# Kernel tuning notes

Measured on AMD Instinct MI355X. Metric: run time of the kernel, lower is better.

## Reference

```python
import jax, jax.numpy as jnp
import numpy as np

NUM_IMGS = 8192
NUM_CAPS = 8192
R = 7        # views per image
D = 256      # embedding dim


def setup_inputs() -> dict:
    key = jax.random.key(0)
    k1, k2 = jax.random.split(key)
    imgs = jax.random.normal(k1, (NUM_IMGS, R, D), dtype=jnp.float32)
    caps = jax.random.normal(k2, (NUM_CAPS, D), dtype=jnp.float32)
    return {"imgs": imgs, "caps": caps}


def reference(imgs, caps):
    # scores[i, r, c] = <imgs[i, r], caps[c]>  then max over views r
    # matches torch.matmul(imgs, caps.t()).max(1)[0]
    scores = jnp.einsum("ird,cd->irc", imgs, caps)  # [num_imgs, r, num_caps]
    return scores.max(axis=1)                        # [num_imgs, num_caps]
```

## Files before the change

### kernel.cpp

```cpp
#include <hip/hip_runtime.h>
#include <hip/hip_bf16.h>
#include <cstdint>
#include <cstddef>

#define NI 8192
#define NC 8192
#define RV 7
#define DD 256

typedef __bf16  bf16x8 __attribute__((ext_vector_type(8)));
typedef float   f32x4  __attribute__((ext_vector_type(4)));
typedef __fp16  f16x2  __attribute__((ext_vector_type(2)));

#define IMGS_WS_BYTES (16u * 56u * 32768u)
#define CAPS_WS_OFF   IMGS_WS_BYTES
#define CAPS_WS_BYTES (64u * 65536u)
#define WS_NEEDED     ((size_t)(IMGS_WS_BYTES + CAPS_WS_BYTES))

static __device__ __forceinline__ unsigned pkbf(float x, float y) {
  unsigned a = __float_as_uint(x) + 0x8000u;
  unsigned b = __float_as_uint(y) + 0x8000u;
  return __builtin_amdgcn_perm(b, a, 0x07060302u);
}

static __device__ __forceinline__ void gload16(const void* g, void* l) {
  __builtin_amdgcn_global_load_lds(
      (const __attribute__((address_space(1))) void*)g,
      (__attribute__((address_space(3))) void*)l, 16, 0, 0);
}

__global__ __launch_bounds__(256)
void conv_imgs(const float* __restrict__ imgs, uint4* __restrict__ ws) {
  unsigned T = blockIdx.x * 256u + threadIdx.x;
  unsigned img = T / 224u;
  unsigned rem = T - img * 224u;
  unsigned r  = rem >> 5;
  unsigned ju = rem & 31u;
  const float* s = imgs + ((size_t)img * RV + r) * DD + ju * 8u;
  float4 a = *(const float4*)s;
  float4 b = *(const float4*)(s + 4);
  uint4 v = { pkbf(a.x, a.y), pkbf(a.z, a.w), pkbf(b.x, b.y), pkbf(b.z, b.w) };
  unsigned ib = img >> 9, lrow = img & 511u;
  unsigned j = ju >> 2, u = ju & 3u;
  unsigned t = r * 8u + j;
  unsigned byteoff = (ib * 56u + t) * 32768u + u * 8192u + lrow * 16u;
  ws[byteoff >> 4] = v;
}

__global__ __launch_bounds__(256)
void conv_caps(const float* __restrict__ caps, uint4* __restrict__ ws) {
  unsigned T = blockIdx.x * 256u + threadIdx.x;
  unsigned gr = T >> 5;
  unsigned ju = T & 31u;
  const float* s = caps + (size_t)gr * DD + ju * 8u;
  float4 a = *(const float4*)s;
  float4 b = *(const float4*)(s + 4);
  uint4 v = { pkbf(a.x, a.y), pkbf(a.z, a.w), pkbf(b.x, b.y), pkbf(b.z, b.w) };
  unsigned cb = gr >> 7, row = gr & 127u;
  unsigned j = ju >> 2, u = ju & 3u;
  unsigned byteoff = cb * 65536u + j * 8192u + u * 2048u + row * 16u;
  ws[byteoff >> 4] = v;
}

__global__ __launch_bounds__(512, 2)
void mvm_mfma(const char* __restrict__ wi, const char* __restrict__ wcap,
              float* __restrict__ out)
{
  __shared__ __align__(1024) char lds[131072];
  char* const ldsA = lds;
  char* const ldsB = lds + 65536;

  const int tid  = threadIdx.x;
  const int lane = tid & 63;
  const int wid  = tid >> 6;
  const int wm   = wid >> 1;
  const int wn   = wid & 1;

  const int bid = (int)blockIdx.x;
  const int swz = (bid & 7) * 128 + (bid >> 3);
  const int ib  = swz >> 6;
  const int cb  = swz & 63;

  const char* abase = wi   + (size_t)ib * (56u * 32768u);
  const char* bbase = wcap + (size_t)cb * 65536u;

  #pragma unroll
  for (int l = 0; l < 8; ++l)
    gload16(bbase + l * 8192 + tid * 16, ldsB + l * 8192 + wid * 1024);
  #pragma unroll
  for (int l = 0; l < 4; ++l)
    gload16(abase + l * 8192 + tid * 16, ldsA + l * 8192 + wid * 1024);

  asm volatile("s_waitcnt vmcnt(0)" ::: "memory");
  __builtin_amdgcn_s_barrier();
  asm volatile("" ::: "memory");

  const int lrow = lane & 15;
  const int lu   = lane >> 4;
  const char* const aB = ldsA + lu * 8192 + (wm * 128 + lrow) * 16;
  const char* const bB = ldsB + lu * 2048 + (wn * 64  + lrow) * 16;
  const char* ap = abase + 32768 + tid * 16;

  f16x2 om[8][4][2];
  #pragma unroll
  for (int m = 0; m < 8; ++m)
    #pragma unroll
    for (int n = 0; n < 4; ++n)
      #pragma unroll
      for (int h = 0; h < 2; ++h)
        om[m][n][h] = (f16x2){(__fp16)-65504.f, (__fp16)-65504.f};

  f32x4 acc[8][4];

  for (int r = 0; r < RV; ++r) {
    #pragma unroll
    for (int m = 0; m < 8; ++m)
      #pragma unroll
      for (int n = 0; n < 4; ++n)
        acc[m][n] = (f32x4){0.f, 0.f, 0.f, 0.f};

    #pragma unroll
    for (int j = 0; j < 8; ++j) {
      const int p = j & 1;
      const bool more = (r < RV - 1) || (j < 7);

      if (more) {
        gload16(ap,         ldsA + (p ^ 1) * 32768 + 0 * 8192 + wid * 1024);
        gload16(ap +  8192, ldsA + (p ^ 1) * 32768 + 1 * 8192 + wid * 1024);
        gload16(ap + 16384, ldsA + (p ^ 1) * 32768 + 2 * 8192 + wid * 1024);
        gload16(ap + 24576, ldsA + (p ^ 1) * 32768 + 3 * 8192 + wid * 1024);
        ap += 32768;
      }

      bf16x8 b0 = *(const bf16x8*)(bB + j * 8192 + 0 * 256);
      bf16x8 b1 = *(const bf16x8*)(bB + j * 8192 + 1 * 256);
      bf16x8 b2 = *(const bf16x8*)(bB + j * 8192 + 2 * 256);
      bf16x8 b3 = *(const bf16x8*)(bB + j * 8192 + 3 * 256);
      bf16x8 a0 = *(const bf16x8*)(aB + p * 32768 + 0 * 256);
      bf16x8 a1 = *(const bf16x8*)(aB + p * 32768 + 1 * 256);
      bf16x8 a2 = *(const bf16x8*)(aB + p * 32768 + 2 * 256);
      bf16x8 a3 = *(const bf16x8*)(aB + p * 32768 + 3 * 256);
      bf16x8 a4 = *(const bf16x8*)(aB + p * 32768 + 4 * 256);
      bf16x8 a5 = *(const bf16x8*)(aB + p * 32768 + 5 * 256);
      bf16x8 a6 = *(const bf16x8*)(aB + p * 32768 + 6 * 256);
      bf16x8 a7 = *(const bf16x8*)(aB + p * 32768 + 7 * 256);

      __builtin_amdgcn_s_setprio(1);
      acc[0][0] = __builtin_amdgcn_mfma_f32_16x16x32_bf16(a0, b0, acc[0][0], 0, 0, 0);
      acc[1][0] = __builtin_amdgcn_mfma_f32_16x16x32_bf16(a1, b0, acc[1][0], 0, 0, 0);
      acc[2][0] = __builtin_amdgcn_mfma_f32_16x16x32_bf16(a2, b0, acc[2][0], 0, 0, 0);
      acc[3][0] = __builtin_amdgcn_mfma_f32_16x16x32_bf16(a3, b0, acc[3][0], 0, 0, 0);
      acc[4][0] = __builtin_amdgcn_mfma_f32_16x16x32_bf16(a4, b0, acc[4][0], 0, 0, 0);
      acc[5][0] = __builtin_amdgcn_mfma_f32_16x16x32_bf16(a5, b0, acc[5][0], 0, 0, 0);
      acc[6][0] = __builtin_amdgcn_mfma_f32_16x16x32_bf16(a6, b0, acc[6][0], 0, 0, 0);
      acc[7][0] = __builtin_amdgcn_mfma_f32_16x16x32_bf16(a7, b0, acc[7][0], 0, 0, 0);
      acc[0][1] = __builtin_amdgcn_mfma_f32_16x16x32_bf16(a0, b1, acc[0][1], 0, 0, 0);
      acc[1][1] = __builtin_amdgcn_mfma_f32_16x16x32_bf16(a1, b1, acc[1][1], 0, 0, 0);
      acc[2][1] = __builtin_amdgcn_mfma_f32_16x16x32_bf16(a2, b1, acc[2][1], 0, 0, 0);
      acc[3][1] = __builtin_amdgcn_mfma_f32_16x16x32_bf16(a3, b1, acc[3][1], 0, 0, 0);
      acc[4][1] = __builtin_amdgcn_mfma_f32_16x16x32_bf16(a4, b1, acc[4][1], 0, 0, 0);
      acc[5][1] = __builtin_amdgcn_mfma_f32_16x16x32_bf16(a5, b1, acc[5][1], 0, 0, 0);
      acc[6][1] = __builtin_amdgcn_mfma_f32_16x16x32_bf16(a6, b1, acc[6][1], 0, 0, 0);
      acc[7][1] = __builtin_amdgcn_mfma_f32_16x16x32_bf16(a7, b1, acc[7][1], 0, 0, 0);
      acc[0][2] = __builtin_amdgcn_mfma_f32_16x16x32_bf16(a0, b2, acc[0][2], 0, 0, 0);
      acc[1][2] = __builtin_amdgcn_mfma_f32_16x16x32_bf16(a1, b2, acc[1][2], 0, 0, 0);
      acc[2][2] = __builtin_amdgcn_mfma_f32_16x16x32_bf16(a2, b2, acc[2][2], 0, 0, 0);
      acc[3][2] = __builtin_amdgcn_mfma_f32_16x16x32_bf16(a3, b2, acc[3][2], 0, 0, 0);
      acc[4][2] = __builtin_amdgcn_mfma_f32_16x16x32_bf16(a4, b2, acc[4][2], 0, 0, 0);
      acc[5][2] = __builtin_amdgcn_mfma_f32_16x16x32_bf16(a5, b2, acc[5][2], 0, 0, 0);
      acc[6][2] = __builtin_amdgcn_mfma_f32_16x16x32_bf16(a6, b2, acc[6][2], 0, 0, 0);
      acc[7][2] = __builtin_amdgcn_mfma_f32_16x16x32_bf16(a7, b2, acc[7][2], 0, 0, 0);
      acc[0][3] = __builtin_amdgcn_mfma_f32_16x16x32_bf16(a0, b3, acc[0][3], 0, 0, 0);
      acc[1][3] = __builtin_amdgcn_mfma_f32_16x16x32_bf16(a1, b3, acc[1][3], 0, 0, 0);
      acc[2][3] = __builtin_amdgcn_mfma_f32_16x16x32_bf16(a2, b3, acc[2][3], 0, 0, 0);
      acc[3][3] = __builtin_amdgcn_mfma_f32_16x16x32_bf16(a3, b3, acc[3][3], 0, 0, 0);
      acc[4][3] = __builtin_amdgcn_mfma_f32_16x16x32_bf16(a4, b3, acc[4][3], 0, 0, 0);
      acc[5][3] = __builtin_amdgcn_mfma_f32_16x16x32_bf16(a5, b3, acc[5][3], 0, 0, 0);
      acc[6][3] = __builtin_amdgcn_mfma_f32_16x16x32_bf16(a6, b3, acc[6][3], 0, 0, 0);
      acc[7][3] = __builtin_amdgcn_mfma_f32_16x16x32_bf16(a7, b3, acc[7][3], 0, 0, 0);
      __builtin_amdgcn_s_setprio(0);

      if (more) {
        asm volatile("s_waitcnt vmcnt(0)" ::: "memory");
        __builtin_amdgcn_s_barrier();
        asm volatile("" ::: "memory");
      }
    }

    #pragma unroll
    for (int m = 0; m < 8; ++m)
      #pragma unroll
      for (int n = 0; n < 4; ++n) {
        f16x2 lo = __builtin_amdgcn_cvt_pkrtz(acc[m][n][0], acc[m][n][1]);
        f16x2 hi = __builtin_amdgcn_cvt_pkrtz(acc[m][n][2], acc[m][n][3]);
        om[m][n][0] = __builtin_elementwise_max(om[m][n][0], lo);
        om[m][n][1] = __builtin_elementwise_max(om[m][n][1], hi);
      }
  }

  const int rbase = ib * 512 + wm * 128;
  const int cbase = cb * 128 + wn * 64;
  #pragma unroll
  for (int m = 0; m < 8; ++m)
    #pragma unroll
    for (int h = 0; h < 2; ++h)
      #pragma unroll
      for (int e = 0; e < 2; ++e) {
        size_t ro = (size_t)(rbase + m * 16 + lu * 4 + h * 2 + e) * NC + cbase + lrow;
        #pragma unroll
        for (int n = 0; n < 4; ++n)
          out[ro + n * 16] = (float)om[m][n][h][e];
      }
}

__global__ __launch_bounds__(512, 1)
void mvm_fallback(const float* __restrict__ imgs, const float* __restrict__ caps,
                  float* __restrict__ out)
{
  __shared__ __align__(16) char ldsB[128 * 512];
  __shared__ __align__(16) char ldsA[2][256 * 128];

  const int tid  = threadIdx.x;
  const int lane = tid & 63;
  const int wid  = tid >> 6;
  const int wr   = wid >> 1;
  const int wc   = wid & 1;
  const int i0   = blockIdx.y * 256;
  const int c0   = blockIdx.x * 128;

  #pragma unroll
  for (int it = 0; it < 8; ++it) {
    int c    = tid + it * 512;
    int row  = c >> 5;
    int colb = (c & 31) * 16;
    const float* p = caps + (size_t)(c0 + row) * DD + (c & 31) * 8;
    float4 a = *(const float4*)p;
    float4 b = *(const float4*)(p + 4);
    uint4 v;
    v.x = pkbf(a.x, a.y); v.y = pkbf(a.z, a.w);
    v.z = pkbf(b.x, b.y); v.w = pkbf(b.z, b.w);
    *(uint4*)(ldsB + row * 512 + (colb ^ ((row & 7) << 4))) = v;
  }
  #pragma unroll
  for (int it = 0; it < 4; ++it) {
    int c    = tid + it * 512;
    int row  = c >> 3;
    int colb = (c & 7) * 16;
    const float* p = imgs + ((size_t)(i0 + row) * RV + 0) * DD + (c & 7) * 8;
    float4 a = *(const float4*)p;
    float4 b = *(const float4*)(p + 4);
    uint4 v;
    v.x = pkbf(a.x, a.y); v.y = pkbf(a.z, a.w);
    v.z = pkbf(b.x, b.y); v.w = pkbf(b.z, b.w);
    *(uint4*)(ldsA[0] + row * 128 + (colb ^ ((row & 7) << 4))) = v;
  }
  __syncthreads();

  f32x4 omax[4][4];
  #pragma unroll
  for (int m = 0; m < 4; ++m)
    #pragma unroll
    for (int n = 0; n < 4; ++n)
      #pragma unroll
      for (int j = 0; j < 4; ++j)
        omax[m][n][j] = -3.4e38f;

  f32x4 acc[4][4];
  int cur = 0;
  const int lrow = lane & 15;
  const int lkb  = (lane >> 4) * 16;

  for (int ch = 0; ch < RV * 4; ++ch) {
    const int kc = ch & 3;
    if (kc == 0) {
      #pragma unroll
      for (int m = 0; m < 4; ++m)
        #pragma unroll
        for (int n = 0; n < 4; ++n)
          acc[m][n] = (f32x4){0.f, 0.f, 0.f, 0.f};
    }
    const int  chn  = ch + 1;
    const bool hasn = (chn < RV * 4);
    float4 pf[8];
    if (hasn) {
      const int rn = chn >> 2;
      const int kn = (chn & 3) * 64;
      #pragma unroll
      for (int it = 0; it < 4; ++it) {
        int c   = tid + it * 512;
        int row = c >> 3;
        const float* p = imgs + ((size_t)(i0 + row) * RV + rn) * DD + kn + (c & 7) * 8;
        pf[2 * it]     = *(const float4*)p;
        pf[2 * it + 1] = *(const float4*)(p + 4);
      }
    }
    #pragma unroll
    for (int ks = 0; ks < 2; ++ks) {
      bf16x8 af[4], bfr[4];
      #pragma unroll
      for (int m = 0; m < 4; ++m) {
        int row = wr * 64 + m * 16 + lrow;
        af[m] = *(const bf16x8*)(ldsA[cur] + row * 128 + ((ks * 64 + lkb) ^ ((row & 7) << 4)));
      }
      #pragma unroll
      for (int n = 0; n < 4; ++n) {
        int row = wc * 64 + n * 16 + lrow;
        bfr[n] = *(const bf16x8*)(ldsB + row * 512 + (((ch & 3) * 128 + ks * 64 + lkb) ^ ((row & 7) << 4)));
      }
      #pragma unroll
      for (int m = 0; m < 4; ++m)
        #pragma unroll
        for (int n = 0; n < 4; ++n)
          acc[m][n] = __builtin_amdgcn_mfma_f32_16x16x32_bf16(af[m], bfr[n], acc[m][n], 0, 0, 0);
    }
    if (hasn) {
      #pragma unroll
      for (int it = 0; it < 4; ++it) {
        int c    = tid + it * 512;
        int row  = c >> 3;
        int colb = (c & 7) * 16;
        uint4 v;
        v.x = pkbf(pf[2 * it].x,     pf[2 * it].y);
        v.y = pkbf(pf[2 * it].z,     pf[2 * it].w);
        v.z = pkbf(pf[2 * it + 1].x, pf[2 * it + 1].y);
        v.w = pkbf(pf[2 * it + 1].z, pf[2 * it + 1].w);
        *(uint4*)(ldsA[cur ^ 1] + row * 128 + (colb ^ ((row & 7) << 4))) = v;
      }
    }
    __syncthreads();
    cur ^= 1;
    if (kc == 3) {
      #pragma unroll
      for (int m = 0; m < 4; ++m)
        #pragma unroll
        for (int n = 0; n < 4; ++n)
          #pragma unroll
          for (int j = 0; j < 4; ++j)
            omax[m][n][j] = fmaxf(omax[m][n][j], acc[m][n][j]);
    }
  }

  const int rbase = i0 + wr * 64;
  const int cbase = c0 + wc * 64;
  const int lr4   = (lane >> 4) * 4;
  const int lc    = lane & 15;
  #pragma unroll
  for (int m = 0; m < 4; ++m)
    #pragma unroll
    for (int j = 0; j < 4; ++j) {
      size_t ro = (size_t)(rbase + m * 16 + lr4 + j) * NC;
      #pragma unroll
      for (int n = 0; n < 4; ++n)
        out[ro + cbase + n * 16 + lc] = omax[m][n][j];
    }
}

extern "C" void kernel_launch(void* const* d_in, const int* in_sizes, int n_in,
                              void* d_out, int out_size, void* d_ws, size_t ws_size,
                              hipStream_t stream) {
  const float* imgs = (const float*)d_in[0];
  const float* caps = (const float*)d_in[1];
  float* out = (float*)d_out;

  if (ws_size >= WS_NEEDED) {
    char* ws = (char*)d_ws;
    conv_imgs<<<7168, 256, 0, stream>>>(imgs, (uint4*)ws);
    conv_caps<<<1024, 256, 0, stream>>>(caps, (uint4*)(ws + CAPS_WS_OFF));
    mvm_mfma<<<1024, 512, 0, stream>>>((const char*)ws, (const char*)(ws + CAPS_WS_OFF), out);
  } else {
    dim3 grid(NC / 128, NI / 256);
    mvm_fallback<<<grid, 512, 0, stream>>>(imgs, caps, out);
  }
}
```

Baseline: 258.8 us.

## Load image operand directly from global into registers, dropping LDS staging

The image (A) tiles are no longer copied into a double-buffered LDS region. Each wave now reads its A fragments straight from the pre-packed global workspace into registers, prefetching the next chunk in two halves between MFMA groups. This removes the per-chunk vmcnt wait and block barrier, and halves the LDS footprint, which may allow two blocks per CU. In exchange, the two waves sharing the same rows duplicate global reads and rely on caches. Load latency is hidden only by a single register-level prefetch stage, and the final prefetch reads past the tile into the next region.

```diff
diff --git a/kernel.cpp b/kernel.cpp
--- a/kernel.cpp
+++ b/kernel.cpp
@@ -66,9 +66,7 @@
 void mvm_mfma(const char* __restrict__ wi, const char* __restrict__ wcap,
               float* __restrict__ out)
 {
-  __shared__ __align__(1024) char lds[131072];
-  char* const ldsA = lds;
-  char* const ldsB = lds + 65536;
+  __shared__ __align__(1024) char ldsB[65536];
 
   const int tid  = threadIdx.x;
   const int lane = tid & 63;
@@ -87,19 +85,24 @@
   #pragma unroll
   for (int l = 0; l < 8; ++l)
     gload16(bbase + l * 8192 + tid * 16, ldsB + l * 8192 + wid * 1024);
-  #pragma unroll
-  for (int l = 0; l < 4; ++l)
-    gload16(abase + l * 8192 + tid * 16, ldsA + l * 8192 + wid * 1024);
-
   asm volatile("s_waitcnt vmcnt(0)" ::: "memory");
   __builtin_amdgcn_s_barrier();
   asm volatile("" ::: "memory");
 
   const int lrow = lane & 15;
   const int lu   = lane >> 4;
-  const char* const aB = ldsA + lu * 8192 + (wm * 128 + lrow) * 16;
-  const char* const bB = ldsB + lu * 2048 + (wn * 64  + lrow) * 16;
-  const char* ap = abase + 32768 + tid * 16;
+  const char* ap = abase + lu * 8192 + (wm * 128 + lrow) * 16;
+  const char* const bB = ldsB + lu * 2048 + (wn * 64 + lrow) * 16;
+
+  bf16x8 p0 = *(const bf16x8*)(ap + 0 * 256);
+  bf16x8 p1 = *(const bf16x8*)(ap + 1 * 256);
+  bf16x8 p2 = *(const bf16x8*)(ap + 2 * 256);
+  bf16x8 p3 = *(const bf16x8*)(ap + 3 * 256);
+  bf16x8 p4 = *(const bf16x8*)(ap + 4 * 256);
+  bf16x8 p5 = *(const bf16x8*)(ap + 5 * 256);
+  bf16x8 p6 = *(const bf16x8*)(ap + 6 * 256);
+  bf16x8 p7 = *(const bf16x8*)(ap + 7 * 256);
+  ap += 32768;
 
   f16x2 om[8][4][2];
   #pragma unroll
@@ -112,6 +115,7 @@
 
   f32x4 acc[8][4];
 
+  #pragma unroll 1
   for (int r = 0; r < RV; ++r) {
     #pragma unroll
     for (int m = 0; m < 8; ++m)
@@ -121,70 +125,55 @@
 
     #pragma unroll
     for (int j = 0; j < 8; ++j) {
-      const int p = j & 1;
-      const bool more = (r < RV - 1) || (j < 7);
-
-      if (more) {
-        gload16(ap,         ldsA + (p ^ 1) * 32768 + 0 * 8192 + wid * 1024);
-        gload16(ap +  8192, ldsA + (p ^ 1) * 32768 + 1 * 8192 + wid * 1024);
-        gload16(ap + 16384, ldsA + (p ^ 1) * 32768 + 2 * 8192 + wid * 1024);
-        gload16(ap + 24576, ldsA + (p ^ 1) * 32768 + 3 * 8192 + wid * 1024);
-        ap += 32768;
-      }
-
       bf16x8 b0 = *(const bf16x8*)(bB + j * 8192 + 0 * 256);
       bf16x8 b1 = *(const bf16x8*)(bB + j * 8192 + 1 * 256);
       bf16x8 b2 = *(const bf16x8*)(bB + j * 8192 + 2 * 256);
       bf16x8 b3 = *(const bf16x8*)(bB + j * 8192 + 3 * 256);
-      bf16x8 a0 = *(const bf16x8*)(aB + p * 32768 + 0 * 256);
-      bf16x8 a1 = *(const bf16x8*)(aB + p * 32768 + 1 * 256);
-      bf16x8 a2 = *(const bf16x8*)(aB + p * 32768 + 2 * 256);
-      bf16x8 a3 = *(const bf16x8*)(aB + p * 32768 + 3 * 256);
-      bf16x8 a4 = *(const bf16x8*)(aB + p * 32768 + 4 * 256);
-      bf16x8 a5 = *(const bf16x8*)(aB + p * 32768 + 5 * 256);
-      bf16x8 a6 = *(const bf16x8*)(aB + p * 32768 + 6 * 256);
-      bf16x8 a7 = *(const bf16x8*)(aB + p * 32768 + 7 * 256);
-
-      __builtin_amdgcn_s_setprio(1);
-      acc[0][0] = __builtin_amdgcn_mfma_f32_16x16x32_bf16(a0, b0, acc[0][0], 0, 0, 0);
-      acc[1][0] = __builtin_amdgcn_mfma_f32_16x16x32_bf16(a1, b0, acc[1][0], 0, 0, 0);
-      acc[2][0] = __builtin_amdgcn_mfma_f32_16x16x32_bf16(a2, b0, acc[2][0], 0, 0, 0);
-      acc[3][0] = __builtin_amdgcn_mfma_f32_16x16x32_bf16(a3, b0, acc[3][0], 0, 0, 0);
-      acc[4][0] = __builtin_amdgcn_mfma_f32_16x16x32_bf16(a4, b0, acc[4][0], 0, 0, 0);
-      acc[5][0] = __builtin_amdgcn_mfma_f32_16x16x32_bf16(a5, b0, acc[5][0], 0, 0, 0);
-      acc[6][0] = __builtin_amdgcn_mfma_f32_16x16x32_bf16(a6, b0, acc[6][0], 0, 0, 0);
-      acc[7][0] = __builtin_amdgcn_mfma_f32_16x16x32_bf16(a7, b0, acc[7][0], 0, 0, 0);
-      acc[0][1] = __builtin_amdgcn_mfma_f32_16x16x32_bf16(a0, b1, acc[0][1], 0, 0, 0);
-      acc[1][1] = __builtin_amdgcn_mfma_f32_16x16x32_bf16(a1, b1, acc[1][1], 0, 0, 0);
-      acc[2][1] = __builtin_amdgcn_mfma_f32_16x16x32_bf16(a2, b1, acc[2][1], 0, 0, 0);
-      acc[3][1] = __builtin_amdgcn_mfma_f32_16x16x32_bf16(a3, b1, acc[3][1], 0, 0, 0);
-      acc[4][1] = __builtin_amdgcn_mfma_f32_16x16x32_bf16(a4, b1, acc[4][1], 0, 0, 0);
-      acc[5][1] = __builtin_amdgcn_mfma_f32_16x16x32_bf16(a5, b1, acc[5][1], 0, 0, 0);
-      acc[6][1] = __builtin_amdgcn_mfma_f32_16x16x32_bf16(a6, b1, acc[6][1], 0, 0, 0);
-      acc[7][1] = __builtin_amdgcn_mfma_f32_16x16x32_bf16(a7, b1, acc[7][1], 0, 0, 0);
-      acc[0][2] = __builtin_amdgcn_mfma_f32_16x16x32_bf16(a0, b2, acc[0][2], 0, 0, 0);
-      acc[1][2] = __builtin_amdgcn_mfma_f32_16x16x32_bf16(a1, b2, acc[1][2], 0, 0, 0);
-      acc[2][2] = __builtin_amdgcn_mfma_f32_16x16x32_bf16(a2, b2, acc[2][2], 0, 0, 0);
-      acc[3][2] = __builtin_amdgcn_mfma_f32_16x16x32_bf16(a3, b2, acc[3][2], 0, 0, 0);
-      acc[4][2] = __builtin_amdgcn_mfma_f32_16x16x32_bf16(a4, b2, acc[4][2], 0, 0, 0);
-      acc[5][2] = __builtin_amdgcn_mfma_f32_16x16x32_bf16(a5, b2, acc[5][2], 0, 0, 0);
-      acc[6][2] = __builtin_amdgcn_mfma_f32_16x16x32_bf16(a6, b2, acc[6][2], 0, 0, 0);
-      acc[7][2] = __builtin_amdgcn_mfma_f32_16x16x32_bf16(a7, b2, acc[7][2], 0, 0, 0);
-      acc[0][3] = __builtin_amdgcn_mfma_f32_16x16x32_bf16(a0, b3, acc[0][3], 0, 0, 0);
-      acc[1][3] = __builtin_amdgcn_mfma_f32_16x16x32_bf16(a1, b3, acc[1][3], 0, 0, 0);
-      acc[2][3] = __builtin_amdgcn_mfma_f32_16x16x32_bf16(a2, b3, acc[2][3], 0, 0, 0);
-      acc[3][3] = __builtin_amdgcn_mfma_f32_16x16x32_bf16(a3, b3, acc[3][3], 0, 0, 0);
-      acc[4][3] = __builtin_amdgcn_mfma_f32_16x16x32_bf16(a4, b3, acc[4][3], 0, 0, 0);
-      acc[5][3] = __builtin_amdgcn_mfma_f32_16x16x32_bf16(a5, b3, acc[5][3], 0, 0, 0);
-      acc[6][3] = __builtin_amdgcn_mfma_f32_16x16x32_bf16(a6, b3, acc[6][3], 0, 0, 0);
-      acc[7][3] = __builtin_amdgcn_mfma_f32_16x16x32_bf16(a7, b3, acc[7][3], 0, 0, 0);
-      __builtin_amdgcn_s_setprio(0);
-
-      if (more) {
-        asm volatile("s_waitcnt vmcnt(0)" ::: "memory");
-        __builtin_amdgcn_s_barrier();
-        asm volatile("" ::: "memory");
-      }
+
+      acc[0][0] = __builtin_amdgcn_mfma_f32_16x16x32_bf16(p0, b0, acc[0][0], 0, 0, 0);
+      acc[1][0] = __builtin_amdgcn_mfma_f32_16x16x32_bf16(p1, b0, acc[1][0], 0, 0, 0);
+      acc[2][0] = __builtin_amdgcn_mfma_f32_16x16x32_bf16(p2, b0, acc[2][0], 0, 0, 0);
+      acc[3][0] = __builtin_amdgcn_mfma_f32_16x16x32_bf16(p3, b0, acc[3][0], 0, 0, 0);
+      acc[0][1] = __builtin_amdgcn_mfma_f32_16x16x32_bf16(p0, b1, acc[0][1], 0, 0, 0);
+      acc[1][1] = __builtin_amdgcn_mfma_f32_16x16x32_bf16(p1, b1, acc[1][1], 0, 0, 0);
+      acc[2][1] = __builtin_amdgcn_mfma_f32_16x16x32_bf16(p2, b1, acc[2][1], 0, 0, 0);
+      acc[3][1] = __builtin_amdgcn_mfma_f32_16x16x32_bf16(p3, b1, acc[3][1], 0, 0, 0);
+      acc[0][2] = __builtin_amdgcn_mfma_f32_16x16x32_bf16(p0, b2, acc[0][2], 0, 0, 0);
+      acc[1][2] = __builtin_amdgcn_mfma_f32_16x16x32_bf16(p1, b2, acc[1][2], 0, 0, 0);
+      acc[2][2] = __builtin_amdgcn_mfma_f32_16x16x32_bf16(p2, b2, acc[2][2], 0, 0, 0);
+      acc[3][2] = __builtin_amdgcn_mfma_f32_16x16x32_bf16(p3, b2, acc[3][2], 0, 0, 0);
+      acc[0][3] = __builtin_amdgcn_mfma_f32_16x16x32_bf16(p0, b3, acc[0][3], 0, 0, 0);
+      acc[1][3] = __builtin_amdgcn_mfma_f32_16x16x32_bf16(p1, b3, acc[1][3], 0, 0, 0);
+      acc[2][3] = __builtin_amdgcn_mfma_f32_16x16x32_bf16(p2, b3, acc[2][3], 0, 0, 0);
+      acc[3][3] = __builtin_amdgcn_mfma_f32_16x16x32_bf16(p3, b3, acc[3][3], 0, 0, 0);
+
+      p0 = *(const bf16x8*)(ap + 0 * 256);
+      p1 = *(const bf16x8*)(ap + 1 * 256);
+      p2 = *(const bf16x8*)(ap + 2 * 256);
+      p3 = *(const bf16x8*)(ap + 3 * 256);
+
+      acc[4][0] = __builtin_amdgcn_mfma_f32_16x16x32_bf16(p4, b0, acc[4][0], 0, 0, 0);
+      acc[5][0] = __builtin_amdgcn_mfma_f32_16x16x32_bf16(p5, b0, acc[5][0], 0, 0, 0);
+      acc[6][0] = __builtin_amdgcn_mfma_f32_16x16x32_bf16(p6, b0, acc[6][0], 0, 0, 0);
+      acc[7][0] = __builtin_amdgcn_mfma_f32_16x16x32_bf16(p7, b0, acc[7][0], 0, 0, 0);
+      acc[4][1] = __builtin_amdgcn_mfma_f32_16x16x32_bf16(p4, b1, acc[4][1], 0, 0, 0);
+      acc[5][1] = __builtin_amdgcn_mfma_f32_16x16x32_bf16(p5, b1, acc[5][1], 0, 0, 0);
+      acc[6][1] = __builtin_amdgcn_mfma_f32_16x16x32_bf16(p6, b1, acc[6][1], 0, 0, 0);
+      acc[7][1] = __builtin_amdgcn_mfma_f32_16x16x32_bf16(p7, b1, acc[7][1], 0, 0, 0);
+      acc[4][2] = __builtin_amdgcn_mfma_f32_16x16x32_bf16(p4, b2, acc[4][2], 0, 0, 0);
+      acc[5][2] = __builtin_amdgcn_mfma_f32_16x16x32_bf16(p5, b2, acc[5][2], 0, 0, 0);
+      acc[6][2] = __builtin_amdgcn_mfma_f32_16x16x32_bf16(p6, b2, acc[6][2], 0, 0, 0);
+      acc[7][2] = __builtin_amdgcn_mfma_f32_16x16x32_bf16(p7, b2, acc[7][2], 0, 0, 0);
+      acc[4][3] = __builtin_amdgcn_mfma_f32_16x16x32_bf16(p4, b3, acc[4][3], 0, 0, 0);
+      acc[5][3] = __builtin_amdgcn_mfma_f32_16x16x32_bf16(p5, b3, acc[5][3], 0, 0, 0);
+      acc[6][3] = __builtin_amdgcn_mfma_f32_16x16x32_bf16(p6, b3, acc[6][3], 0, 0, 0);
+      acc[7][3] = __builtin_amdgcn_mfma_f32_16x16x32_bf16(p7, b3, acc[7][3], 0, 0, 0);
+
+      p4 = *(const bf16x8*)(ap + 4 * 256);
+      p5 = *(const bf16x8*)(ap + 5 * 256);
+      p6 = *(const bf16x8*)(ap + 6 * 256);
+      p7 = *(const bf16x8*)(ap + 7 * 256);
+      ap += 32768;
     }
 
     #pragma unroll
```

New measurement: 860.3 us. 3.32x slower.

## Halve image tile to 256 rows and single-buffer A with 4-wave blocks

Applied to the files above, without the earlier changes.

Shrinks each workgroup to 4 waves covering 256 image rows by 128 captions, with 2048 blocks instead of 1024, and re-lays the image workspace to 256-row blocks. The A operand changes from double-buffered LDS to a single 16 KB buffer: fragments are read into registers, a barrier follows, and the next chunk's loads are issued before the MFMAs, so LDS drops to 80 KB per block. The aim is to fit more blocks per CU and overlap loads with MFMA using less shared memory. In exchange each step has an extra barrier, and the caption tile is reloaded by twice as many blocks.

```diff
diff --git a/kernel.cpp b/kernel.cpp
--- a/kernel.cpp
+++ b/kernel.cpp
@@ -12,7 +12,7 @@
 typedef float   f32x4  __attribute__((ext_vector_type(4)));
 typedef __fp16  f16x2  __attribute__((ext_vector_type(2)));
 
-#define IMGS_WS_BYTES (16u * 56u * 32768u)
+#define IMGS_WS_BYTES (32u * 56u * 16384u)
 #define CAPS_WS_OFF   IMGS_WS_BYTES
 #define CAPS_WS_BYTES (64u * 65536u)
 #define WS_NEEDED     ((size_t)(IMGS_WS_BYTES + CAPS_WS_BYTES))
@@ -40,10 +40,10 @@
   float4 a = *(const float4*)s;
   float4 b = *(const float4*)(s + 4);
   uint4 v = { pkbf(a.x, a.y), pkbf(a.z, a.w), pkbf(b.x, b.y), pkbf(b.z, b.w) };
-  unsigned ib = img >> 9, lrow = img & 511u;
+  unsigned ib = img >> 8, lrow = img & 255u;
   unsigned j = ju >> 2, u = ju & 3u;
   unsigned t = r * 8u + j;
-  unsigned byteoff = (ib * 56u + t) * 32768u + u * 8192u + lrow * 16u;
+  unsigned byteoff = (ib * 56u + t) * 16384u + u * 4096u + lrow * 16u;
   ws[byteoff >> 4] = v;
 }
 
@@ -62,13 +62,13 @@
   ws[byteoff >> 4] = v;
 }
 
-__global__ __launch_bounds__(512, 2)
+__global__ __launch_bounds__(256, 2)
 void mvm_mfma(const char* __restrict__ wi, const char* __restrict__ wcap,
               float* __restrict__ out)
 {
-  __shared__ __align__(1024) char lds[131072];
-  char* const ldsA = lds;
-  char* const ldsB = lds + 65536;
+  __shared__ __align__(1024) char lds[81920];
+  char* const ldsB = lds;
+  char* const ldsA = lds + 65536;
 
   const int tid  = threadIdx.x;
   const int lane = tid & 63;
@@ -77,29 +77,28 @@
   const int wn   = wid & 1;
 
   const int bid = (int)blockIdx.x;
-  const int swz = (bid & 7) * 128 + (bid >> 3);
+  const int swz = (bid & 7) * 256 + (bid >> 3);
   const int ib  = swz >> 6;
   const int cb  = swz & 63;
 
-  const char* abase = wi   + (size_t)ib * (56u * 32768u);
+  const char* abase = wi   + (size_t)ib * (56u * 16384u);
   const char* bbase = wcap + (size_t)cb * 65536u;
 
   #pragma unroll
-  for (int l = 0; l < 8; ++l)
-    gload16(bbase + l * 8192 + tid * 16, ldsB + l * 8192 + wid * 1024);
+  for (int l = 0; l < 16; ++l)
+    gload16(bbase + l * 4096 + tid * 16, ldsB + l * 4096 + wid * 1024);
   #pragma unroll
   for (int l = 0; l < 4; ++l)
-    gload16(abase + l * 8192 + tid * 16, ldsA + l * 8192 + wid * 1024);
-
+    gload16(abase + l * 4096 + tid * 16, ldsA + l * 4096 + wid * 1024);
   asm volatile("s_waitcnt vmcnt(0)" ::: "memory");
   __builtin_amdgcn_s_barrier();
   asm volatile("" ::: "memory");
 
   const int lrow = lane & 15;
   const int lu   = lane >> 4;
-  const char* const aB = ldsA + lu * 8192 + (wm * 128 + lrow) * 16;
-  const char* const bB = ldsB + lu * 2048 + (wn * 64  + lrow) * 16;
-  const char* ap = abase + 32768 + tid * 16;
+  const char* const aB = ldsA + lu * 4096 + (wm * 128 + lrow) * 16;
+  const char* const bB = ldsB + lu * 2048 + (wn * 64 + lrow) * 16;
+  const char* ap = abase + 16384 + tid * 16;
 
   f16x2 om[8][4][2];
   #pragma unroll
@@ -112,6 +111,7 @@
 
   f32x4 acc[8][4];
 
+  #pragma unroll 1
   for (int r = 0; r < RV; ++r) {
     #pragma unroll
     for (int m = 0; m < 8; ++m)
@@ -121,29 +121,31 @@
 
     #pragma unroll
     for (int j = 0; j < 8; ++j) {
-      const int p = j & 1;
-      const bool more = (r < RV - 1) || (j < 7);
-
-      if (more) {
-        gload16(ap,         ldsA + (p ^ 1) * 32768 + 0 * 8192 + wid * 1024);
-        gload16(ap +  8192, ldsA + (p ^ 1) * 32768 + 1 * 8192 + wid * 1024);
-        gload16(ap + 16384, ldsA + (p ^ 1) * 32768 + 2 * 8192 + wid * 1024);
-        gload16(ap + 24576, ldsA + (p ^ 1) * 32768 + 3 * 8192 + wid * 1024);
-        ap += 32768;
-      }
-
       bf16x8 b0 = *(const bf16x8*)(bB + j * 8192 + 0 * 256);
       bf16x8 b1 = *(const bf16x8*)(bB + j * 8192 + 1 * 256);
       bf16x8 b2 = *(const bf16x8*)(bB + j * 8192 + 2 * 256);
       bf16x8 b3 = *(const bf16x8*)(bB + j * 8192 + 3 * 256);
-      bf16x8 a0 = *(const bf16x8*)(aB + p * 32768 + 0 * 256);
-      bf16x8 a1 = *(const bf16x8*)(aB + p * 32768 + 1 * 256);
-      bf16x8 a2 = *(const bf16x8*)(aB + p * 32768 + 2 * 256);
-      bf16x8 a3 = *(const bf16x8*)(aB + p * 32768 + 3 * 256);
-      bf16x8 a4 = *(const bf16x8*)(aB + p * 32768 + 4 * 256);
-      bf16x8 a5 = *(const bf16x8*)(aB + p * 32768 + 5 * 256);
-      bf16x8 a6 = *(const bf16x8*)(aB + p * 32768 + 6 * 256);
-      bf16x8 a7 = *(const bf16x8*)(aB + p * 32768 + 7 * 256);
+      bf16x8 a0 = *(const bf16x8*)(aB + 0 * 256);
+      bf16x8 a1 = *(const bf16x8*)(aB + 1 * 256);
+      bf16x8 a2 = *(const bf16x8*)(aB + 2 * 256);
+      bf16x8 a3 = *(const bf16x8*)(aB + 3 * 256);
+      bf16x8 a4 = *(const bf16x8*)(aB + 4 * 256);
+      bf16x8 a5 = *(const bf16x8*)(aB + 5 * 256);
+      bf16x8 a6 = *(const bf16x8*)(aB + 6 * 256);
+      bf16x8 a7 = *(const bf16x8*)(aB + 7 * 256);
+
+      asm volatile("s_waitcnt lgkmcnt(0)" ::: "memory");
+      __builtin_amdgcn_s_barrier();
+      asm volatile("" ::: "memory");
+
+      if (j < 7 || r < RV - 1) {
+        gload16(ap + 0 * 4096, ldsA + 0 * 4096 + wid * 1024);
+        gload16(ap + 1 * 4096, ldsA + 1 * 4096 + wid * 1024);
+        gload16(ap + 2 * 4096, ldsA + 2 * 4096 + wid * 1024);
+        gload16(ap + 3 * 4096, ldsA + 3 * 4096 + wid * 1024);
+        ap += 16384;
+      }
+      __builtin_amdgcn_sched_barrier(0);
 
       __builtin_amdgcn_s_setprio(1);
       acc[0][0] = __builtin_amdgcn_mfma_f32_16x16x32_bf16(a0, b0, acc[0][0], 0, 0, 0);
@@ -180,11 +182,9 @@
       acc[7][3] = __builtin_amdgcn_mfma_f32_16x16x32_bf16(a7, b3, acc[7][3], 0, 0, 0);
       __builtin_amdgcn_s_setprio(0);
 
-      if (more) {
-        asm volatile("s_waitcnt vmcnt(0)" ::: "memory");
-        __builtin_amdgcn_s_barrier();
-        asm volatile("" ::: "memory");
-      }
+      asm volatile("s_waitcnt vmcnt(0)" ::: "memory");
+      __builtin_amdgcn_s_barrier();
+      asm volatile("" ::: "memory");
     }
 
     #pragma unroll
@@ -198,7 +198,7 @@
       }
   }
 
-  const int rbase = ib * 512 + wm * 128;
+  const int rbase = ib * 256 + wm * 128;
   const int cbase = cb * 128 + wn * 64;
   #pragma unroll
   for (int m = 0; m < 8; ++m)
@@ -366,7 +366,7 @@
     char* ws = (char*)d_ws;
     conv_imgs<<<7168, 256, 0, stream>>>(imgs, (uint4*)ws);
     conv_caps<<<1024, 256, 0, stream>>>(caps, (uint4*)(ws + CAPS_WS_OFF));
-    mvm_mfma<<<1024, 512, 0, stream>>>((const char*)ws, (const char*)(ws + CAPS_WS_OFF), out);
+    mvm_mfma<<<2048, 256, 0, stream>>>((const char*)ws, (const char*)(ws + CAPS_WS_OFF), out);
   } else {
     dim3 grid(NC / 128, NI / 256);
     mvm_fallback<<<grid, 512, 0, stream>>>(imgs, caps, out);
```

Result: slower. 338.4 us (+30.8%).
